# Performance work log

Hardware: AMD Instinct MI355X
Metric: run time of the kernel (lower is better)

The kernel has to match this reference:

```python
import jax, jax.numpy as jnp
import numpy as np

B, S, Hd, NH, FF = 4, 2048, 1024, 16, 4096
D = Hd // NH  # head size 64
EPS = 1e-12


def _ln(x, g, b):
    mu = jnp.mean(x, axis=-1, keepdims=True)
    var = jnp.mean(jnp.square(x - mu), axis=-1, keepdims=True)
    return (x - mu) * jax.lax.rsqrt(var + EPS) * g + b


def _rope(q, k):
    # q,k: [B,NH,S,D]; RoFormer interleaved rotary
    inv = 1.0 / (10000.0 ** (jnp.arange(0, D, 2, dtype=jnp.float32) / D))
    freqs = jnp.arange(S, dtype=jnp.float32)[:, None] * inv[None, :]  # [S,D/2]
    cos = jnp.repeat(jnp.cos(freqs), 2, axis=-1)  # [S,D]
    sin = jnp.repeat(jnp.sin(freqs), 2, axis=-1)

    def rot(x):  # [x0,x1,x2,x3,...] -> [-x1,x0,-x3,x2,...]
        return jnp.stack([-x[..., 1::2], x[..., 0::2]], axis=-1).reshape(x.shape)

    return q * cos + rot(q) * sin, k * cos + rot(k) * sin


def setup_inputs() -> dict:
    key = jax.random.key(0)
    ks = jax.random.split(key, 12)
    s = 0.02
    return {
        "x": jax.random.normal(ks[0], (B, S, Hd), jnp.float32),
        "Wq": jax.random.normal(ks[1], (Hd, Hd), jnp.float32) * s,
        "bq": jnp.zeros((Hd,), jnp.float32),
        "Wk": jax.random.normal(ks[2], (Hd, Hd), jnp.float32) * s,
        "bk": jnp.zeros((Hd,), jnp.float32),
        "Wv": jax.random.normal(ks[3], (Hd, Hd), jnp.float32) * s,
        "bv": jnp.zeros((Hd,), jnp.float32),
        "Wo": jax.random.normal(ks[4], (Hd, Hd), jnp.float32) * s,
        "bo": jnp.zeros((Hd,), jnp.float32),
        "g1": jnp.ones((Hd,), jnp.float32),
        "beta1": jnp.zeros((Hd,), jnp.float32),
        "W1": jax.random.normal(ks[5], (Hd, FF), jnp.float32) * s,
        "b1": jnp.zeros((FF,), jnp.float32),
        "W2": jax.random.normal(ks[6], (FF, Hd), jnp.float32) * s,
        "b2": jnp.zeros((Hd,), jnp.float32),
        "g2": jnp.ones((Hd,), jnp.float32),
        "beta2": jnp.zeros((Hd,), jnp.float32),
    }


def reference(x, Wq, bq, Wk, bk, Wv, bv, Wo, bo, g1, beta1, W1, b1, W2, b2, g2, beta2):
    def proj(W, b):  # [B,S,Hd] -> [B,NH,S,D]
        return (x @ W + b).reshape(B, S, NH, D).transpose(0, 2, 1, 3)

    q, k, v = proj(Wq, bq), proj(Wk, bk), proj(Wv, bv)
    q, k = _rope(q, k)
    scores = jnp.einsum('bhqd,bhkd->bhqk', q, k) / jnp.sqrt(jnp.float32(D))
    attn = jax.nn.softmax(scores, axis=-1)
    ctx = jnp.einsum('bhqk,bhkd->bhqd', attn, v)
    ctx = ctx.transpose(0, 2, 1, 3).reshape(B, S, Hd)
    attn_out = ctx @ Wo + bo
    h = _ln(x + attn_out, g1, beta1)
    ffn = jax.nn.gelu(h @ W1 + b1) @ W2 + b2
    return _ln(h + ffn, g2, beta2)
```

## Files before the change

kernel.cpp:

```cpp
#include <hip/hip_runtime.h>

#define BB   4
#define SS   2048
#define HD   1024
#define NHH  16
#define DD   64
#define FFF  4096
#define BS   (BB*SS)
#define BHN  (BB*NHH)

typedef __attribute__((ext_vector_type(8))) short v8s;
typedef __attribute__((ext_vector_type(4))) short v4s;
typedef __attribute__((ext_vector_type(4))) float v4f;

__device__ __forceinline__ short f2bf(float f) {
    union { float f; unsigned u; } v; v.f = f;
    unsigned r = (v.u + 0x7fffu + ((v.u >> 16) & 1u)) >> 16;
    return (short)r;
}
__device__ __forceinline__ float bf2f(short s) {
    union { unsigned u; float f; } v; v.u = ((unsigned)(unsigned short)s) << 16;
    return v.f;
}
__device__ __forceinline__ unsigned pktrunc(float lo, float hi) {
    return __builtin_amdgcn_perm(__builtin_bit_cast(unsigned, hi),
                                 __builtin_bit_cast(unsigned, lo), 0x07060302u);
}
__device__ __forceinline__ v4f mfma16(v8s a, v8s b, v4f c) {
    return __builtin_amdgcn_mfma_f32_16x16x32_bf16(a, b, c, 0, 0, 0);
}
__device__ __forceinline__ void cp16(void* lds, const void* g) {
    __builtin_amdgcn_global_load_lds(
        (const __attribute__((address_space(1))) unsigned*)g,
        (__attribute__((address_space(3))) unsigned*)lds, 16, 0, 0);
}


__global__ __launch_bounds__(256) void cast_bf16(const float* __restrict__ X,
                                                 short* __restrict__ Y, int n) {
    const int i = (blockIdx.x * 256 + threadIdx.x) * 4;
    if (i < n) {
        const float4 v = *(const float4*)(X + i);
        v4s o = { f2bf(v.x), f2bf(v.y), f2bf(v.z), f2bf(v.w) };
        *(v4s*)(Y + i) = o;
    }
}

__global__ __launch_bounds__(256) void rope_tab(float* __restrict__ C, float* __restrict__ Sn) {
    const int i = blockIdx.x * 256 + threadIdx.x;
    const int s = i >> 5, di = i & 31;
    const float inv = powf(10000.f, -(float)(2 * di) * (1.f / 64.f));
    const float a = (float)s * inv;
    C[i]  = cosf(a);
    Sn[i] = sinf(a);
}

__global__ __launch_bounds__(256) void transW_all(
    const float* __restrict__ Wq, const float* __restrict__ Wk,
    const float* __restrict__ Wv, const float* __restrict__ Wo,
    const float* __restrict__ W1, const float* __restrict__ W2,
    short* __restrict__ WqkvT, short* __restrict__ WoT,
    short* __restrict__ W1T, short* __restrict__ W2T)
{
    const int id = blockIdx.x;
    const float* W; short* WT; int K, N, bx, by;
    if (id < 768) {
        const int m = id >> 8;
        W = (m == 0) ? Wq : (m == 1) ? Wk : Wv;
        WT = WqkvT + (size_t)m * HD * HD;
        K = HD; N = HD; const int r = id & 255; bx = r & 15; by = r >> 4;
    } else if (id < 1024) {
        W = Wo; WT = WoT; K = HD; N = HD;
        const int r = id - 768; bx = r & 15; by = r >> 4;
    } else if (id < 2048) {
        W = W1; WT = W1T; K = HD; N = FFF;
        const int r = id - 1024; bx = r & 63; by = r >> 6;
    } else {
        W = W2; WT = W2T; K = FFF; N = HD;
        const int r = id - 2048; bx = r & 15; by = r >> 4;
    }
    __shared__ float T[64][65];
    const int t = threadIdx.x;
    const int r0 = by * 64, c0 = bx * 64;
#pragma unroll
    for (int i = 0; i < 4; i++) {
        const int lin = t + 256 * i;
        const int r = lin >> 4, c = (lin & 15) * 4;
        const float4 v = *(const float4*)(W + (size_t)(r0 + r) * N + c0 + c);
        T[r][c] = v.x; T[r][c+1] = v.y; T[r][c+2] = v.z; T[r][c+3] = v.w;
    }
    __syncthreads();
#pragma unroll
    for (int i = 0; i < 4; i++) {
        const int lin = t + 256 * i;
        const int n = lin >> 4, k = (lin & 15) * 4;
        v4s o = { f2bf(T[k][n]), f2bf(T[k+1][n]), f2bf(T[k+2][n]), f2bf(T[k+3][n]) };
        *(v4s*)(WT + (size_t)(c0 + n) * K + r0 + k) = o;
    }
}


template <int EPI>
__global__ __launch_bounds__(256, 2) void gemm128(
    const short* __restrict__ A, const short* __restrict__ Bt,
    const float* __restrict__ bias, const float* __restrict__ bias2,
    const float* __restrict__ bias3, void* __restrict__ out,
    void* __restrict__ out2, const void* __restrict__ resid,
    const float* __restrict__ ropeC, const float* __restrict__ ropeS,
    int M, int N, int K, float oscale)
{
    __shared__ short As[2][128 * 64];
    __shared__ short Bs[2][128 * 64];
    const int t = threadIdx.x;
    const int wave = t >> 6, lane = t & 63;
    const int quad = lane >> 4, l16 = lane & 15;
    const int wm = wave & 1, wn = wave >> 1;
    const int m0 = blockIdx.x * 128, n0 = blockIdx.y * 128;

    v4f acc[4][4];
#pragma unroll
    for (int i = 0; i < 4; i++)
#pragma unroll
        for (int j = 0; j < 4; j++) { v4f z = {0.f, 0.f, 0.f, 0.f}; acc[i][j] = z; }

    const int r8 = lane >> 3;
    const int g8 = (lane & 7) ^ r8;
    const short* Asrc = A  + (size_t)(m0 + wave * 32 + r8) * K + g8 * 8;
    const short* Bsrc = Bt + (size_t)(n0 + wave * 32 + r8) * K + g8 * 8;
    const int wofs = wave * 2048;
    const int xsw = l16 & 7;

    auto stage = [&](int buf, int kofs) {
#pragma unroll
        for (int s = 0; s < 4; s++) {
            cp16(&As[buf][wofs + s * 512], Asrc + (size_t)(s * 8) * K + kofs);
            cp16(&Bs[buf][wofs + s * 512], Bsrc + (size_t)(s * 8) * K + kofs);
        }
    };

    stage(0, 0);
    __syncthreads();

    int cur = 0;
    for (int k0 = 0; k0 < K; k0 += 64) {
        if (k0 + 64 < K) stage(cur ^ 1, k0 + 64);
#pragma unroll
        for (int ks = 0; ks < 2; ks++) {
            v8s af[4], bfr[4];
#pragma unroll
            for (int i = 0; i < 4; i++)
                af[i] = *(const v8s*)(&As[cur][(wm * 64 + i * 16 + l16) * 64
                                              + ((ks * 4 + quad) ^ xsw) * 8]);
#pragma unroll
            for (int j = 0; j < 4; j++)
                bfr[j] = *(const v8s*)(&Bs[cur][(wn * 64 + j * 16 + l16) * 64
                                               + ((ks * 4 + quad) ^ xsw) * 8]);
#pragma unroll
            for (int i = 0; i < 4; i++)
#pragma unroll
                for (int j = 0; j < 4; j++)
                    acc[i][j] = mfma16(af[i], bfr[j], acc[i][j]);
        }
        __syncthreads();
        cur ^= 1;
    }

#pragma unroll
    for (int j = 0; j < 4; j++) {
        const int col = n0 + wn * 64 + j * 16 + l16;
        if constexpr (EPI == 0) {
            const int h = col >> 10;
            const float* bp = (h == 0) ? bias : ((h == 1) ? bias2 : bias3);
            const float bval = bp[col & 1023];
            const int d = col & 63;
            const int hh = (col >> 6) & 15;
            if (h == 2) {
#pragma unroll
                for (int i = 0; i < 4; i++) {
                    const int row0 = m0 + wm * 64 + i * 16 + quad * 4;
                    const int b_ = row0 >> 11, s0 = row0 & (SS - 1);
                    v4s ov = { f2bf(acc[i][j][0] + bval), f2bf(acc[i][j][1] + bval),
                               f2bf(acc[i][j][2] + bval), f2bf(acc[i][j][3] + bval) };
                    *(v4s*)((short*)out2 + ((size_t)(b_ * NHH + hh) * DD + d) * SS + s0) = ov;
                }
            } else {
#pragma unroll
                for (int i = 0; i < 4; i++) {
#pragma unroll
                    for (int r = 0; r < 4; r++) {
                        const int row = m0 + wm * 64 + i * 16 + quad * 4 + r;
                        float v = acc[i][j][r] + bval;
                        if (h == 0) v *= oscale;
                        const int s = row & (SS - 1);
                        const float cv = ropeC[s * 32 + (d >> 1)];
                        const float sv = ropeS[s * 32 + (d >> 1)];
                        const float partner = __shfl_xor(v, 1);
                        const float o = (d & 1) ? fmaf(v, cv, partner * sv)
                                                : fmaf(v, cv, -partner * sv);
                        const int b_ = row >> 11;
                        ((short*)out)[(size_t)h * (BHN * SS * DD)
                                      + (((size_t)(b_ * NHH + hh)) * SS + s) * DD + d] = f2bf(o);
                    }
                }
            }
        } else if constexpr (EPI == 3) {
            const float bval = bias[col];
#pragma unroll
            for (int i = 0; i < 4; i++) {
#pragma unroll
                for (int r = 0; r < 4; r++) {
                    const int row = m0 + wm * 64 + i * 16 + quad * 4 + r;
                    float v = acc[i][j][r] + bval;
                    const float tq = v * v;
                    const float u = v * fmaf(0.035677408136f, tq, 0.7978845608028654f);
                    const float e = __builtin_amdgcn_exp2f(-2.8853900817779268f * u);
                    const float g = v * __builtin_amdgcn_rcpf(1.f + e);
                    ((short*)out)[(size_t)row * N + col] = f2bf(g);
                }
            }
        } else {
            const float bval = bias[col];
#pragma unroll
            for (int i = 0; i < 4; i++) {
#pragma unroll
                for (int r = 0; r < 4; r++) {
                    const int row = m0 + wm * 64 + i * 16 + quad * 4 + r;
                    float v = acc[i][j][r] + bval;
                    if constexpr (EPI == 2) v += ((const float*)resid)[(size_t)row * N + col];
                    else                    v += bf2f(((const short*)resid)[(size_t)row * N + col]);
                    ((float*)out)[(size_t)row * N + col] = v;
                }
            }
        }
    }
}

__global__ __launch_bounds__(256, 4) void attn_kernel(
    const short* __restrict__ Qh, const short* __restrict__ Kh,
    const short* __restrict__ Vt, short* __restrict__ ctx)
{
    __shared__ short Ks[64 * 64];
    __shared__ short Vs[64 * 64];
    __shared__ short Ps[4][16 * 88];
    __shared__ float Li[4][32];
    const int bh = blockIdx.x, q0 = blockIdx.y * 128;
    const int t = threadIdx.x, wave = t >> 6, lane = t & 63;
    const int quad = lane >> 4, l16 = lane & 15;

    const short* qp = Qh + ((size_t)bh * SS + q0 + wave * 32 + l16) * DD;
    v8s bq[2][2];
    bq[0][0] = *(const v8s*)(qp + quad * 8);
    bq[0][1] = *(const v8s*)(qp + 32 + quad * 8);
    bq[1][0] = *(const v8s*)(qp + (size_t)16 * DD + quad * 8);
    bq[1][1] = *(const v8s*)(qp + (size_t)16 * DD + 32 + quad * 8);

    v4f o[2][4];
#pragma unroll
    for (int qs = 0; qs < 2; qs++)
#pragma unroll
        for (int c = 0; c < 4; c++) { v4f z = {0.f, 0.f, 0.f, 0.f}; o[qs][c] = z; }
    float li[2] = {0.f, 0.f};

    const short* Kb = Kh + (size_t)bh * SS * DD;
    const short* Vb = Vt + (size_t)bh * DD * SS;
    const int r8 = lane >> 3;
    const int g8 = (lane & 7) ^ (r8 & 7);
    short* Psw = (short*)Ps[wave];
    const int xsw = l16 & 7;

    for (int kt = 0; kt < SS; kt += 64) {
        __syncthreads();
        cp16(Ks + wave * 1024,       Kb + (size_t)(kt + wave * 16 + r8) * DD + g8 * 8);
        cp16(Ks + wave * 1024 + 512, Kb + (size_t)(kt + wave * 16 + 8 + r8) * DD + g8 * 8);
        cp16(Vs + wave * 1024,       Vb + (size_t)(wave * 16 + r8) * SS + kt + g8 * 8);
        cp16(Vs + wave * 1024 + 512, Vb + (size_t)(wave * 16 + 8 + r8) * SS + kt + g8 * 8);
        __syncthreads();

        v4f sc[2][4];
#pragma unroll
        for (int c = 0; c < 4; c++) {
            const v8s k0f = *(const v8s*)(Ks + (c * 16 + l16) * 64 + ((quad    ) ^ xsw) * 8);
            const v8s k1f = *(const v8s*)(Ks + (c * 16 + l16) * 64 + ((quad + 4) ^ xsw) * 8);
#pragma unroll
            for (int qs = 0; qs < 2; qs++) {
                v4f z = {0.f, 0.f, 0.f, 0.f};
                z = mfma16(k0f, bq[qs][0], z);
                z = mfma16(k1f, bq[qs][1], z);
                sc[qs][c] = z;
            }
        }

        v8s pa[2][2];
#pragma unroll
        for (int qs = 0; qs < 2; qs++) {
            float lp = 0.f;
#pragma unroll
            for (int c = 0; c < 4; c++) {
#pragma unroll
                for (int r = 0; r < 4; r++) {
                    const float p = __builtin_amdgcn_exp2f(sc[qs][c][r]);
                    sc[qs][c][r] = p;
                    lp += p;
                }
            }
            li[qs] += lp;
            short* pw = Psw + l16 * 88;
#pragma unroll
            for (int c = 0; c < 4; c++) {
                uint2 w;
                w.x = pktrunc(sc[qs][c][0], sc[qs][c][1]);
                w.y = pktrunc(sc[qs][c][2], sc[qs][c][3]);
                *(uint2*)(pw + c * 16 + quad * 4) = w;
            }
            pa[qs][0] = *(const v8s*)(Psw + l16 * 88 + quad * 8);
            pa[qs][1] = *(const v8s*)(Psw + l16 * 88 + 32 + quad * 8);
        }

#pragma unroll
        for (int c = 0; c < 4; c++) {
            const v8s v0f = *(const v8s*)(Vs + (c * 16 + l16) * 64 + ((quad    ) ^ xsw) * 8);
            const v8s v1f = *(const v8s*)(Vs + (c * 16 + l16) * 64 + ((quad + 4) ^ xsw) * 8);
#pragma unroll
            for (int qs = 0; qs < 2; qs++) {
                o[qs][c] = mfma16(pa[qs][0], v0f, o[qs][c]);
                o[qs][c] = mfma16(pa[qs][1], v1f, o[qs][c]);
            }
        }
    }

    float linv[2][4];
#pragma unroll
    for (int qs = 0; qs < 2; qs++) {
        float lf = li[qs];
        lf += __shfl_xor(lf, 16);
        lf += __shfl_xor(lf, 32);
        if (quad == 0) Li[wave][qs * 16 + l16] = lf;
    }
    __syncthreads();
#pragma unroll
    for (int qs = 0; qs < 2; qs++) {
        const v4f lv = *(const v4f*)(&Li[wave][qs * 16 + quad * 4]);
#pragma unroll
        for (int r = 0; r < 4; r++) linv[qs][r] = __builtin_amdgcn_rcpf(lv[r]);
    }
    const int b_ = bh >> 4, h_ = bh & 15;
#pragma unroll
    for (int qs = 0; qs < 2; qs++)
#pragma unroll
        for (int c = 0; c < 4; c++)
#pragma unroll
            for (int r = 0; r < 4; r++) {
                const int s = q0 + wave * 32 + qs * 16 + quad * 4 + r;
                const int d = c * 16 + l16;
                ctx[((size_t)(b_ * SS + s)) * HD + h_ * DD + d] =
                    f2bf(o[qs][c][r] * linv[qs][r]);
            }
}

__global__ __launch_bounds__(256) void ln_kernel(
    const float* __restrict__ X, const float* __restrict__ g, const float* __restrict__ b,
    float* __restrict__ Y, short* __restrict__ Yb)
{
    const int row = blockIdx.x;
    const int t = threadIdx.x;
    const float4 v = *(const float4*)(X + (size_t)row * HD + t * 4);
    float s = v.x + v.y + v.z + v.w;
    float sq = v.x * v.x + v.y * v.y + v.z * v.z + v.w * v.w;
#pragma unroll
    for (int m = 1; m < 64; m <<= 1) { s += __shfl_xor(s, m); sq += __shfl_xor(sq, m); }
    __shared__ float red[8];
    const int wave = t >> 6, lane = t & 63;
    if (lane == 0) { red[wave] = s; red[4 + wave] = sq; }
    __syncthreads();
    s  = red[0] + red[1] + red[2] + red[3];
    sq = red[4] + red[5] + red[6] + red[7];
    const float mu = s * (1.f / HD);
    const float var = sq * (1.f / HD) - mu * mu;
    const float rs = rsqrtf(var + 1e-12f);
    const float4 gg = *(const float4*)(g + t * 4);
    const float4 bb = *(const float4*)(b + t * 4);
    const float y0 = (v.x - mu) * rs * gg.x + bb.x;
    const float y1 = (v.y - mu) * rs * gg.y + bb.y;
    const float y2 = (v.z - mu) * rs * gg.z + bb.z;
    const float y3 = (v.w - mu) * rs * gg.w + bb.w;
    if (Y)  { float4 o = { y0, y1, y2, y3 }; *(float4*)(Y + (size_t)row * HD + t * 4) = o; }
    if (Yb) { v4s o = { f2bf(y0), f2bf(y1), f2bf(y2), f2bf(y3) };
              *(v4s*)(Yb + (size_t)row * HD + t * 4) = o; }
}

extern "C" void kernel_launch(void* const* d_in, const int* in_sizes, int n_in,
                              void* d_out, int out_size, void* d_ws, size_t ws_size,
                              hipStream_t stream)
{
    (void)in_sizes; (void)n_in; (void)out_size;
    const float* x   = (const float*)d_in[0];
    const float* Wq  = (const float*)d_in[1];
    const float* bq  = (const float*)d_in[2];
    const float* Wk  = (const float*)d_in[3];
    const float* bk  = (const float*)d_in[4];
    const float* Wv  = (const float*)d_in[5];
    const float* bv  = (const float*)d_in[6];
    const float* Wo  = (const float*)d_in[7];
    const float* bo  = (const float*)d_in[8];
    const float* g1  = (const float*)d_in[9];
    const float* be1 = (const float*)d_in[10];
    const float* W1  = (const float*)d_in[11];
    const float* b1  = (const float*)d_in[12];
    const float* W2  = (const float*)d_in[13];
    const float* b2  = (const float*)d_in[14];
    const float* g2  = (const float*)d_in[15];
    const float* be2 = (const float*)d_in[16];

    char* ws = (char*)d_ws;
    size_t off = 0;
    auto alloc = [&](size_t sz) { char* p = ws + off; off += sz; return p; };
    short* xb    = (short*)alloc((size_t)BS * HD * 2);
    short* WqkvT = (short*)alloc((size_t)3 * HD * HD * 2);
    short* WoT   = (short*)alloc((size_t)HD * HD * 2);
    short* W1T   = (short*)alloc((size_t)FFF * HD * 2);
    short* W2T   = (short*)alloc((size_t)HD * FFF * 2);
    float* ropeC = (float*)alloc((size_t)SS * 32 * 4);
    float* ropeS = (float*)alloc((size_t)SS * 32 * 4);
    short* Qh    = (short*)alloc((size_t)BHN * SS * DD * 2);
    short* Kh    = (short*)alloc((size_t)BHN * SS * DD * 2);
    short* Vt    = (short*)alloc((size_t)BHN * SS * DD * 2);
    short* ctx   = (short*)alloc((size_t)BS * HD * 2);
    float* ao    = (float*)alloc((size_t)BS * HD * 4);
    if (off > ws_size) return;
    short* f1 = Qh;
    short* hb = xb;
    float* f2 = (float*)d_out;

    const float qsc = 0.125f * 1.4426950408889634f;

    cast_bf16<<<BS * HD / 1024, 256, 0, stream>>>(x, xb, BS * HD);
    rope_tab<<<SS * 32 / 256, 256, 0, stream>>>(ropeC, ropeS);
    transW_all<<<3072, 256, 0, stream>>>(Wq, Wk, Wv, Wo, W1, W2,
                                         WqkvT, WoT, W1T, W2T);

    gemm128<0><<<dim3(64, 24), 256, 0, stream>>>(xb, WqkvT, bq, bk, bv, Qh, Vt,
                                                 nullptr, ropeC, ropeS, BS, 3 * HD, HD, qsc);
    attn_kernel<<<dim3(64, SS / 128), 256, 0, stream>>>(Qh, Kh, Vt, ctx);
    gemm128<2><<<dim3(64, 8), 256, 0, stream>>>(ctx, WoT, bo, nullptr, nullptr, ao,
                                                nullptr, x, nullptr, nullptr, BS, HD, HD, 1.0f);
    ln_kernel<<<BS, 256, 0, stream>>>(ao, g1, be1, nullptr, hb);
    gemm128<3><<<dim3(64, 32), 256, 0, stream>>>(hb, W1T, b1, nullptr, nullptr, f1,
                                                 nullptr, nullptr, nullptr, nullptr, BS, FFF, HD, 1.0f);
    gemm128<4><<<dim3(64, 8), 256, 0, stream>>>(f1, W2T, b2, nullptr, nullptr, f2,
                                                nullptr, hb, nullptr, nullptr, BS, HD, FFF, 1.0f);
    ln_kernel<<<BS, 256, 0, stream>>>(f2, g2, be2, (float*)d_out, nullptr);
}
```

Before: 497.9 us.

## Deepen GEMM pipeline to four K=32 LDS stages with partial vmcnt waits

The 128x128 bf16 GEMM now uses four LDS buffers of K=32 instead of two of K=64, and issues async copies two tiles ahead. It waits with partial vmcnt counters instead of draining all loads before each barrier, so more global loads stay in flight while the MFMAs run. A new XOR swizzle fits the narrower rows. The cost is twice as many barriers per K and fewer MFMAs between barriers. The hand-counted waits are correct only if the compiler issues no other vector memory ops inside the loop.

```diff
diff --git a/kernel.cpp b/kernel.cpp
--- a/kernel.cpp
+++ b/kernel.cpp
@@ -109,10 +109,10 @@
     const float* __restrict__ ropeC, const float* __restrict__ ropeS,
     int M, int N, int K, float oscale)
 {
-    __shared__ short As[2][128 * 64];
-    __shared__ short Bs[2][128 * 64];
-    const int t = threadIdx.x;
-    const int wave = t >> 6, lane = t & 63;
+    __shared__ short As[4][128 * 32];
+    __shared__ short Bs[4][128 * 32];
+    const int tid = threadIdx.x;
+    const int wave = tid >> 6, lane = tid & 63;
     const int quad = lane >> 4, l16 = lane & 15;
     const int wm = wave & 1, wn = wave >> 1;
     const int m0 = blockIdx.x * 128, n0 = blockIdx.y * 128;
@@ -123,46 +123,46 @@
 #pragma unroll
         for (int j = 0; j < 4; j++) { v4f z = {0.f, 0.f, 0.f, 0.f}; acc[i][j] = z; }
 
-    const int r8 = lane >> 3;
-    const int g8 = (lane & 7) ^ r8;
-    const short* Asrc = A  + (size_t)(m0 + wave * 32 + r8) * K + g8 * 8;
-    const short* Bsrc = Bt + (size_t)(n0 + wave * 32 + r8) * K + g8 * 8;
-    const int wofs = wave * 2048;
-    const int xsw = l16 & 7;
+    const int r4 = lane >> 2;
+    const int g4 = (lane & 3) ^ ((lane >> 3) & 3);
+    const short* Asrc = A  + (size_t)(m0 + wave * 32 + r4) * K + g4 * 8;
+    const short* Bsrc = Bt + (size_t)(n0 + wave * 32 + r4) * K + g4 * 8;
+    const int pshift = (l16 >> 1) & 3;
 
     auto stage = [&](int buf, int kofs) {
-#pragma unroll
-        for (int s = 0; s < 4; s++) {
-            cp16(&As[buf][wofs + s * 512], Asrc + (size_t)(s * 8) * K + kofs);
-            cp16(&Bs[buf][wofs + s * 512], Bsrc + (size_t)(s * 8) * K + kofs);
-        }
+        cp16(&As[buf][wave * 1024],       Asrc + kofs);
+        cp16(&As[buf][wave * 1024 + 512], Asrc + (size_t)16 * K + kofs);
+        cp16(&Bs[buf][wave * 1024],       Bsrc + kofs);
+        cp16(&Bs[buf][wave * 1024 + 512], Bsrc + (size_t)16 * K + kofs);
     };
 
     stage(0, 0);
-    __syncthreads();
-
-    int cur = 0;
-    for (int k0 = 0; k0 < K; k0 += 64) {
-        if (k0 + 64 < K) stage(cur ^ 1, k0 + 64);
-#pragma unroll
-        for (int ks = 0; ks < 2; ks++) {
-            v8s af[4], bfr[4];
-#pragma unroll
-            for (int i = 0; i < 4; i++)
-                af[i] = *(const v8s*)(&As[cur][(wm * 64 + i * 16 + l16) * 64
-                                              + ((ks * 4 + quad) ^ xsw) * 8]);
+    stage(1, 32);
+    asm volatile("s_waitcnt vmcnt(4)" ::: "memory");
+    __builtin_amdgcn_s_barrier();
+
+    const int NT = K >> 5;
+    for (int it = 0; it < NT; ++it) {
+        const int cur = it & 3;
+        const bool more = (it + 2) < NT;
+        if (more) stage((it + 2) & 3, (it + 2) << 5);
+        v8s af[4], bfr[4];
+#pragma unroll
+        for (int i = 0; i < 4; i++)
+            af[i] = *(const v8s*)(&As[cur][(wm * 64 + i * 16 + l16) * 32
+                                           + (quad ^ pshift) * 8]);
+#pragma unroll
+        for (int j = 0; j < 4; j++)
+            bfr[j] = *(const v8s*)(&Bs[cur][(wn * 64 + j * 16 + l16) * 32
+                                            + (quad ^ pshift) * 8]);
+#pragma unroll
+        for (int i = 0; i < 4; i++)
 #pragma unroll
             for (int j = 0; j < 4; j++)
-                bfr[j] = *(const v8s*)(&Bs[cur][(wn * 64 + j * 16 + l16) * 64
-                                               + ((ks * 4 + quad) ^ xsw) * 8]);
-#pragma unroll
-            for (int i = 0; i < 4; i++)
-#pragma unroll
-                for (int j = 0; j < 4; j++)
-                    acc[i][j] = mfma16(af[i], bfr[j], acc[i][j]);
-        }
-        __syncthreads();
-        cur ^= 1;
+                acc[i][j] = mfma16(af[i], bfr[j], acc[i][j]);
+        if (more) asm volatile("s_waitcnt vmcnt(4)" ::: "memory");
+        else      asm volatile("s_waitcnt vmcnt(0)" ::: "memory");
+        __builtin_amdgcn_s_barrier();
     }
 
 #pragma unroll
```

Measured after the change: 551.2 us. +10.7%, slower.

## Stage GEMM epilogues through LDS for coalesced stores; merge prep kernels

Applied to the files above, without the earlier changes.

The GEMM epilogues now write results into a shared LDS buffer that reuses the A/B tiles, synchronize, and then issue wide 16-byte coalesced global stores. Previously each lane wrote scattered 2- or 4-byte values, including a transposed V layout. The residual add in the fp32 epilogues is also vectorized. Separately, the cast, rope-table and weight-transpose kernels are merged into one launch to cut launch overhead. The cost is an extra barrier per block and LDS traffic in the epilogue.

```diff
diff --git a/kernel.cpp b/kernel.cpp
--- a/kernel.cpp
+++ b/kernel.cpp
@@ -35,52 +35,51 @@
         (__attribute__((address_space(3))) unsigned*)lds, 16, 0, 0);
 }
 
-
-__global__ __launch_bounds__(256) void cast_bf16(const float* __restrict__ X,
-                                                 short* __restrict__ Y, int n) {
-    const int i = (blockIdx.x * 256 + threadIdx.x) * 4;
-    if (i < n) {
-        const float4 v = *(const float4*)(X + i);
-        v4s o = { f2bf(v.x), f2bf(v.y), f2bf(v.z), f2bf(v.w) };
-        *(v4s*)(Y + i) = o;
-    }
-}
-
-__global__ __launch_bounds__(256) void rope_tab(float* __restrict__ C, float* __restrict__ Sn) {
-    const int i = blockIdx.x * 256 + threadIdx.x;
-    const int s = i >> 5, di = i & 31;
-    const float inv = powf(10000.f, -(float)(2 * di) * (1.f / 64.f));
-    const float a = (float)s * inv;
-    C[i]  = cosf(a);
-    Sn[i] = sinf(a);
-}
-
-__global__ __launch_bounds__(256) void transW_all(
+__global__ __launch_bounds__(256) void prep_all(
+    const float* __restrict__ x, short* __restrict__ xb,
+    float* __restrict__ ropeC, float* __restrict__ ropeS,
     const float* __restrict__ Wq, const float* __restrict__ Wk,
     const float* __restrict__ Wv, const float* __restrict__ Wo,
     const float* __restrict__ W1, const float* __restrict__ W2,
     short* __restrict__ WqkvT, short* __restrict__ WoT,
     short* __restrict__ W1T, short* __restrict__ W2T)
 {
+    __shared__ float T[64][65];
+    const int t = threadIdx.x;
     const int id = blockIdx.x;
+    if (id < 8192) {
+        const int i = (id * 256 + t) * 4;
+        const float4 v = *(const float4*)(x + i);
+        v4s o = { f2bf(v.x), f2bf(v.y), f2bf(v.z), f2bf(v.w) };
+        *(v4s*)(xb + i) = o;
+        return;
+    }
+    if (id < 8448) {
+        const int i = (id - 8192) * 256 + t;
+        const int s = i >> 5, di = i & 31;
+        const float inv = powf(10000.f, -(float)(2 * di) * (1.f / 64.f));
+        const float a = (float)s * inv;
+        ropeC[i] = cosf(a);
+        ropeS[i] = sinf(a);
+        return;
+    }
+    const int wid = id - 8448;
     const float* W; short* WT; int K, N, bx, by;
-    if (id < 768) {
-        const int m = id >> 8;
+    if (wid < 768) {
+        const int m = wid >> 8;
         W = (m == 0) ? Wq : (m == 1) ? Wk : Wv;
         WT = WqkvT + (size_t)m * HD * HD;
-        K = HD; N = HD; const int r = id & 255; bx = r & 15; by = r >> 4;
-    } else if (id < 1024) {
+        K = HD; N = HD; const int r = wid & 255; bx = r & 15; by = r >> 4;
+    } else if (wid < 1024) {
         W = Wo; WT = WoT; K = HD; N = HD;
-        const int r = id - 768; bx = r & 15; by = r >> 4;
-    } else if (id < 2048) {
+        const int r = wid - 768; bx = r & 15; by = r >> 4;
+    } else if (wid < 2048) {
         W = W1; WT = W1T; K = HD; N = FFF;
-        const int r = id - 1024; bx = r & 63; by = r >> 6;
+        const int r = wid - 1024; bx = r & 63; by = r >> 6;
     } else {
         W = W2; WT = W2T; K = FFF; N = HD;
-        const int r = id - 2048; bx = r & 15; by = r >> 4;
-    }
-    __shared__ float T[64][65];
-    const int t = threadIdx.x;
+        const int r = wid - 2048; bx = r & 15; by = r >> 4;
+    }
     const int r0 = by * 64, c0 = bx * 64;
 #pragma unroll
     for (int i = 0; i < 4; i++) {
@@ -109,10 +108,9 @@
     const float* __restrict__ ropeC, const float* __restrict__ ropeS,
     int M, int N, int K, float oscale)
 {
-    __shared__ short As[2][128 * 64];
-    __shared__ short Bs[2][128 * 64];
-    const int t = threadIdx.x;
-    const int wave = t >> 6, lane = t & 63;
+    __shared__ short sh[32768];
+    const int tid = threadIdx.x;
+    const int wave = tid >> 6, lane = tid & 63;
     const int quad = lane >> 4, l16 = lane & 15;
     const int wm = wave & 1, wn = wave >> 1;
     const int m0 = blockIdx.x * 128, n0 = blockIdx.y * 128;
@@ -131,10 +129,12 @@
     const int xsw = l16 & 7;
 
     auto stage = [&](int buf, int kofs) {
+        short* Ad = sh + buf * 8192 + wofs;
+        short* Bd = sh + 16384 + buf * 8192 + wofs;
 #pragma unroll
         for (int s = 0; s < 4; s++) {
-            cp16(&As[buf][wofs + s * 512], Asrc + (size_t)(s * 8) * K + kofs);
-            cp16(&Bs[buf][wofs + s * 512], Bsrc + (size_t)(s * 8) * K + kofs);
+            cp16(Ad + s * 512, Asrc + (size_t)(s * 8) * K + kofs);
+            cp16(Bd + s * 512, Bsrc + (size_t)(s * 8) * K + kofs);
         }
     };
 
@@ -149,12 +149,12 @@
             v8s af[4], bfr[4];
 #pragma unroll
             for (int i = 0; i < 4; i++)
-                af[i] = *(const v8s*)(&As[cur][(wm * 64 + i * 16 + l16) * 64
-                                              + ((ks * 4 + quad) ^ xsw) * 8]);
+                af[i] = *(const v8s*)(&sh[cur * 8192 + (wm * 64 + i * 16 + l16) * 64
+                                          + ((ks * 4 + quad) ^ xsw) * 8]);
 #pragma unroll
             for (int j = 0; j < 4; j++)
-                bfr[j] = *(const v8s*)(&Bs[cur][(wn * 64 + j * 16 + l16) * 64
-                                               + ((ks * 4 + quad) ^ xsw) * 8]);
+                bfr[j] = *(const v8s*)(&sh[16384 + cur * 8192 + (wn * 64 + j * 16 + l16) * 64
+                                           + ((ks * 4 + quad) ^ xsw) * 8]);
 #pragma unroll
             for (int i = 0; i < 4; i++)
 #pragma unroll
@@ -165,72 +165,133 @@
         cur ^= 1;
     }
 
-#pragma unroll
-    for (int j = 0; j < 4; j++) {
-        const int col = n0 + wn * 64 + j * 16 + l16;
-        if constexpr (EPI == 0) {
-            const int h = col >> 10;
-            const float* bp = (h == 0) ? bias : ((h == 1) ? bias2 : bias3);
-            const float bval = bp[col & 1023];
-            const int d = col & 63;
-            const int hh = (col >> 6) & 15;
-            if (h == 2) {
+    if constexpr (EPI == 0) {
+        const int h = n0 >> 10;
+        short* stg = sh;
+        if (h == 2) {
+#pragma unroll
+            for (int j = 0; j < 4; j++) {
+                const int lc = wn * 64 + j * 16 + l16;
+                const float bval = bias3[(n0 + lc) & 1023];
 #pragma unroll
                 for (int i = 0; i < 4; i++) {
-                    const int row0 = m0 + wm * 64 + i * 16 + quad * 4;
-                    const int b_ = row0 >> 11, s0 = row0 & (SS - 1);
+                    const int row0 = wm * 64 + i * 16 + quad * 4;
                     v4s ov = { f2bf(acc[i][j][0] + bval), f2bf(acc[i][j][1] + bval),
                                f2bf(acc[i][j][2] + bval), f2bf(acc[i][j][3] + bval) };
-                    *(v4s*)((short*)out2 + ((size_t)(b_ * NHH + hh) * DD + d) * SS + s0) = ov;
+                    *(v4s*)(stg + lc * 136 + row0) = ov;
                 }
-            } else {
+            }
+            __syncthreads();
+#pragma unroll
+            for (int c8 = 0; c8 < 8; ++c8) {
+                const int lin = c8 * 256 + tid;
+                const int lc = lin >> 4, ch = lin & 15;
+                const int gcol = n0 + lc;
+                const int hh = (gcol >> 6) & 15, d = gcol & 63;
+                const int grow = m0 + ch * 8;
+                const int b_ = grow >> 11, s0 = grow & (SS - 1);
+                const v8s v = *(const v8s*)(stg + lc * 136 + ch * 8);
+                *(v8s*)((short*)out2 + ((size_t)(b_ * NHH + hh) * DD + d) * SS + s0) = v;
+            }
+        } else {
+            const float* bp = (h == 0) ? bias : bias2;
+#pragma unroll
+            for (int j = 0; j < 4; j++) {
+                const int lc = wn * 64 + j * 16 + l16;
+                const int col = n0 + lc;
+                const float bval = bp[col & 1023];
+                const int d = col & 63;
 #pragma unroll
                 for (int i = 0; i < 4; i++) {
 #pragma unroll
                     for (int r = 0; r < 4; r++) {
-                        const int row = m0 + wm * 64 + i * 16 + quad * 4 + r;
+                        const int row = wm * 64 + i * 16 + quad * 4 + r;
                         float v = acc[i][j][r] + bval;
                         if (h == 0) v *= oscale;
-                        const int s = row & (SS - 1);
+                        const int s = (m0 + row) & (SS - 1);
                         const float cv = ropeC[s * 32 + (d >> 1)];
                         const float sv = ropeS[s * 32 + (d >> 1)];
                         const float partner = __shfl_xor(v, 1);
                         const float o = (d & 1) ? fmaf(v, cv, partner * sv)
                                                 : fmaf(v, cv, -partner * sv);
-                        const int b_ = row >> 11;
-                        ((short*)out)[(size_t)h * (BHN * SS * DD)
-                                      + (((size_t)(b_ * NHH + hh)) * SS + s) * DD + d] = f2bf(o);
+                        stg[row * 136 + lc] = f2bf(o);
                     }
                 }
             }
-        } else if constexpr (EPI == 3) {
-            const float bval = bias[col];
+            __syncthreads();
+            const size_t hbase = (size_t)h * (BHN * SS * DD);
+#pragma unroll
+            for (int c8 = 0; c8 < 8; ++c8) {
+                const int lin = c8 * 256 + tid;
+                const int row = lin >> 4, ch = lin & 15;
+                const int grow = m0 + row;
+                const int b_ = grow >> 11, s = grow & (SS - 1);
+                const int gcol = n0 + ch * 8;
+                const int hh = (gcol >> 6) & 15, d = gcol & 63;
+                const v8s v = *(const v8s*)(stg + row * 136 + ch * 8);
+                *(v8s*)((short*)out + hbase
+                        + (((size_t)(b_ * NHH + hh)) * SS + s) * DD + d) = v;
+            }
+        }
+    } else if constexpr (EPI == 3) {
+        short* stg = sh;
+#pragma unroll
+        for (int j = 0; j < 4; j++) {
+            const int lc = wn * 64 + j * 16 + l16;
+            const float bval = bias[n0 + lc];
 #pragma unroll
             for (int i = 0; i < 4; i++) {
 #pragma unroll
                 for (int r = 0; r < 4; r++) {
-                    const int row = m0 + wm * 64 + i * 16 + quad * 4 + r;
+                    const int row = wm * 64 + i * 16 + quad * 4 + r;
                     float v = acc[i][j][r] + bval;
                     const float tq = v * v;
                     const float u = v * fmaf(0.035677408136f, tq, 0.7978845608028654f);
                     const float e = __builtin_amdgcn_exp2f(-2.8853900817779268f * u);
                     const float g = v * __builtin_amdgcn_rcpf(1.f + e);
-                    ((short*)out)[(size_t)row * N + col] = f2bf(g);
+                    stg[row * 136 + lc] = f2bf(g);
                 }
             }
-        } else {
-            const float bval = bias[col];
+        }
+        __syncthreads();
+#pragma unroll
+        for (int c8 = 0; c8 < 8; ++c8) {
+            const int lin = c8 * 256 + tid;
+            const int row = lin >> 4, ch = lin & 15;
+            const v8s v = *(const v8s*)(stg + row * 136 + ch * 8);
+            *(v8s*)((short*)out + (size_t)(m0 + row) * N + n0 + ch * 8) = v;
+        }
+    } else {
+        float* stg = (float*)sh;
+#pragma unroll
+        for (int j = 0; j < 4; j++) {
+            const int lc = wn * 64 + j * 16 + l16;
+            const float bval = bias[n0 + lc];
 #pragma unroll
             for (int i = 0; i < 4; i++) {
 #pragma unroll
                 for (int r = 0; r < 4; r++) {
-                    const int row = m0 + wm * 64 + i * 16 + quad * 4 + r;
-                    float v = acc[i][j][r] + bval;
-                    if constexpr (EPI == 2) v += ((const float*)resid)[(size_t)row * N + col];
-                    else                    v += bf2f(((const short*)resid)[(size_t)row * N + col]);
-                    ((float*)out)[(size_t)row * N + col] = v;
+                    const int row = wm * 64 + i * 16 + quad * 4 + r;
+                    stg[row * 128 + lc] = acc[i][j][r] + bval;
                 }
             }
+        }
+        __syncthreads();
+#pragma unroll
+        for (int c4 = 0; c4 < 16; ++c4) {
+            const int lin = c4 * 256 + tid;
+            const int row = lin >> 5, ch = lin & 31;
+            float4 v = *(const float4*)(stg + row * 128 + ch * 4);
+            const size_t gi = (size_t)(m0 + row) * N + n0 + ch * 4;
+            if constexpr (EPI == 2) {
+                const float4 rv = *(const float4*)((const float*)resid + gi);
+                v.x += rv.x; v.y += rv.y; v.z += rv.z; v.w += rv.w;
+            } else {
+                const v4s rb = *(const v4s*)((const short*)resid + gi);
+                v.x += bf2f(rb[0]); v.y += bf2f(rb[1]);
+                v.z += bf2f(rb[2]); v.w += bf2f(rb[3]);
+            }
+            *(float4*)((float*)out + gi) = v;
         }
     }
 }
@@ -433,10 +494,9 @@
 
     const float qsc = 0.125f * 1.4426950408889634f;
 
-    cast_bf16<<<BS * HD / 1024, 256, 0, stream>>>(x, xb, BS * HD);
-    rope_tab<<<SS * 32 / 256, 256, 0, stream>>>(ropeC, ropeS);
-    transW_all<<<3072, 256, 0, stream>>>(Wq, Wk, Wv, Wo, W1, W2,
-                                         WqkvT, WoT, W1T, W2T);
+    prep_all<<<11520, 256, 0, stream>>>(x, xb, ropeC, ropeS,
+                                        Wq, Wk, Wv, Wo, W1, W2,
+                                        WqkvT, WoT, W1T, W2T);
 
     gemm128<0><<<dim3(64, 24), 256, 0, stream>>>(xb, WqkvT, bq, bk, bv, Qh, Vt,
                                                  nullptr, ropeC, ropeS, BS, 3 * HD, HD, qsc);
```

Result: no change. 503.3 us (+1.1%).
